# Kernel optimization log

Hardware: AMD Instinct MI355X
Metric: run time of the kernel (lower is better)

The kernel has to match this reference:

```python
import jax, jax.numpy as jnp
import numpy as np

N = 2048          # num nodes
C = 256           # dense_dim per input
EMB = 3 * C       # 768
H = 8             # num_heads
D = EMB // H      # 96 head_dim
ALPHA = 0.2       # leaky relu slope
SCALE = D ** -0.5


def setup_inputs() -> dict:
    key = jax.random.key(0)
    ks = jax.random.split(key, 9)
    sd = EMB ** -0.5
    return {
        "eh": jax.random.normal(ks[0], (N, C), jnp.float32),
        "er": jax.random.normal(ks[1], (N, C), jnp.float32),
        "et": jax.random.normal(ks[2], (N, C), jnp.float32),
        "h_id": jax.random.randint(ks[3], (N,), 0, 32),
        "W_w": jax.random.normal(ks[4], (EMB, EMB), jnp.float32) * sd,
        "a": jax.random.normal(ks[5], (2 * D, 1), jnp.float32) * (2 * D) ** -0.5,
        "proj_w": jax.random.normal(ks[6], (EMB, EMB), jnp.float32) * sd,
        "proj_b": jnp.zeros((EMB,), jnp.float32),
        "skip_w": jax.random.normal(ks[7], (EMB, EMB), jnp.float32) * sd,
        "skip_b": jnp.zeros((EMB,), jnp.float32),
    }


def reference(eh, er, et, h_id, W_w, a, proj_w, proj_b, skip_w, skip_b):
    n = eh.shape[0]
    e = jnp.concatenate([eh, er, et], axis=-1)            # [N, EMB]
    Wh = (e @ W_w.T).reshape(n, H, D)                     # [N, H, D]

    # score = leakyrelu(a1 . Wh_scrambled[i] + a2 . Wh[j]) * scale
    a1, a2 = a[:D, 0], a[D:, 0]
    s1 = Wh @ a1                                          # [N, H]
    s2 = Wh @ a2                                          # [N, H]
    # torch's Wh.repeat(1,1,N).view(N*N,H,D) reads head (j*H + h)//N for pair (i,j,h)
    qidx = (jnp.arange(n)[:, None] * H + jnp.arange(H)[None, :]) // n  # [N, H]
    x = s1[:, qidx] + s2[None, :, :]                      # [N, N, H]
    e_ij = jnp.where(x >= 0, x, ALPHA * x) * SCALE

    mask = h_id[:, None] != h_id[None, :]                 # [N, N]
    e_ij = jnp.where(mask[:, :, None], -jnp.inf, e_ij)
    attn = jax.nn.softmax(e_ij, axis=1)                   # softmax over neighbors j

    out = jnp.einsum('ijh,jhd->ihd', attn, Wh).reshape(n, H * D)
    out = out @ proj_w.T + proj_b                         # [N, EMB]
    skip = e @ skip_w.T + skip_b                          # [N, EMB]
    return skip + out
```

## Files before the change

### kernel.cpp

```cpp
#include <hip/hip_runtime.h>
#include <hip/hip_bf16.h>

#define N_NODES 2048
#define EMB 768
#define NH 8
#define DH 96
#define ALPHA 0.2f
#define SCALE 0.10206207261596575f

typedef __bf16 bf16x8 __attribute__((ext_vector_type(8)));
typedef float f32x4 __attribute__((ext_vector_type(4)));
typedef __attribute__((address_space(3))) unsigned int lds_u32;
typedef __attribute__((address_space(1))) const unsigned int glb_u32;

union pack4 { ushort4 u; __hip_bfloat16 h[4]; };

__global__ __launch_bounds__(256) void prep_kernel(
    const float* __restrict__ eh, const float* __restrict__ er, const float* __restrict__ et,
    const float* __restrict__ W0, const float* __restrict__ W1, const float* __restrict__ W2,
    __hip_bfloat16* __restrict__ e, __hip_bfloat16* __restrict__ o0,
    __hip_bfloat16* __restrict__ o1, __hip_bfloat16* __restrict__ o2, int* __restrict__ cnt)
{
    const int b = blockIdx.x;
    const int gtid = b * 256 + threadIdx.x;
    if (gtid < 32) cnt[gtid] = 0;
    const float* src;
    __hip_bfloat16* dst;
    if (b < 1536) {
        int idx = gtid * 4;
        int i = idx / EMB, c = idx % EMB;
        if (c < 256)      src = eh + i * 256 + c;
        else if (c < 512) src = er + i * 256 + (c - 256);
        else              src = et + i * 256 + (c - 512);
        dst = e + (size_t)i * EMB + c;
    } else {
        const int WSZ = EMB * EMB;
        int idx = (gtid - 1536 * 256) * 4;
        if (idx < WSZ)          { src = W0 + idx;           dst = o0 + idx; }
        else if (idx < 2 * WSZ) { src = W1 + idx - WSZ;     dst = o1 + idx - WSZ; }
        else                    { src = W2 + idx - 2 * WSZ; dst = o2 + idx - 2 * WSZ; }
    }
    float4 v = *reinterpret_cast<const float4*>(src);
    pack4 p;
    p.h[0] = __float2bfloat16(v.x);
    p.h[1] = __float2bfloat16(v.y);
    p.h[2] = __float2bfloat16(v.z);
    p.h[3] = __float2bfloat16(v.w);
    *reinterpret_cast<ushort4*>(dst) = p.u;
}

__device__ __forceinline__ void stage_tile(
    const __hip_bfloat16* __restrict__ src, int row0, int k0,
    __hip_bfloat16* lds, int wave, int lane)
{
#pragma unroll
    for (int r = 0; r < 2; r++) {
        const int L = wave * 128 + r * 64 + lane;
        const int row = L >> 3;
        const int cb = (L & 7) ^ (row & 7);
        const __hip_bfloat16* g = src + (size_t)(row0 + row) * EMB + k0 + cb * 8;
        __builtin_amdgcn_global_load_lds(
            (glb_u32*)g, (lds_u32*)(lds + (size_t)(wave * 128 + r * 64) * 8), 16, 0, 0);
    }
}

__global__ __launch_bounds__(256) void gemm_nt_kernel(
    const __hip_bfloat16* __restrict__ A1, const __hip_bfloat16* __restrict__ B1, int ns1,
    const __hip_bfloat16* __restrict__ A2, const __hip_bfloat16* __restrict__ B2, int ns2,
    const float* __restrict__ bias1, const float* __restrict__ bias2,
    float* __restrict__ Cf)
{
    __shared__ __attribute__((aligned(16))) __hip_bfloat16 sm[2][2][4096];

    const int t = threadIdx.x;
    const int lane = t & 63, wave = t >> 6;
    const int wm = wave >> 1, wn = wave & 1;
    const int bm = blockIdx.y * 64, bn = blockIdx.x * 64;
    const int l15 = lane & 15, quad = lane >> 4;
    const int NS = ns1 + ns2;

    f32x4 acc00 = {0.f,0.f,0.f,0.f}, acc01 = {0.f,0.f,0.f,0.f};
    f32x4 acc10 = {0.f,0.f,0.f,0.f}, acc11 = {0.f,0.f,0.f,0.f};

    stage_tile(A1, bm, 0, &sm[0][0][0], wave, lane);
    stage_tile(B1, bn, 0, &sm[0][1][0], wave, lane);

    const int rA = wm * 32 + l15;
    const int rB = wn * 32 + l15;
    const int xa = rA & 7, xb = rB & 7;

    for (int s = 0; s < NS; s++) {
        __syncthreads();
        if (s + 1 < NS) {
            const int sn = s + 1;
            const __hip_bfloat16* As = (sn < ns1) ? A1 : A2;
            const __hip_bfloat16* Bs = (sn < ns1) ? B1 : B2;
            const int k0 = ((sn < ns1) ? sn : sn - ns1) * 64;
            stage_tile(As, bm, k0, &sm[sn & 1][0][0], wave, lane);
            stage_tile(Bs, bn, k0, &sm[sn & 1][1][0], wave, lane);
        }
        const __hip_bfloat16* At = &sm[s & 1][0][0];
        const __hip_bfloat16* Bt = &sm[s & 1][1][0];
#pragma unroll
        for (int ks = 0; ks < 2; ks++) {
            const int cq = ks * 4 + quad;
            bf16x8 a0 = *(const bf16x8*)(At + ((size_t)rA        * 8 + (cq ^ xa)) * 8);
            bf16x8 a1 = *(const bf16x8*)(At + ((size_t)(rA + 16) * 8 + (cq ^ xa)) * 8);
            bf16x8 b0 = *(const bf16x8*)(Bt + ((size_t)rB        * 8 + (cq ^ xb)) * 8);
            bf16x8 b1 = *(const bf16x8*)(Bt + ((size_t)(rB + 16) * 8 + (cq ^ xb)) * 8);
            acc00 = __builtin_amdgcn_mfma_f32_16x16x32_bf16(a0, b0, acc00, 0, 0, 0);
            acc01 = __builtin_amdgcn_mfma_f32_16x16x32_bf16(a0, b1, acc01, 0, 0, 0);
            acc10 = __builtin_amdgcn_mfma_f32_16x16x32_bf16(a1, b0, acc10, 0, 0, 0);
            acc11 = __builtin_amdgcn_mfma_f32_16x16x32_bf16(a1, b1, acc11, 0, 0, 0);
        }
    }

    const int col0 = bn + wn * 32 + l15;
    const int col1 = col0 + 16;
    float bv0 = 0.f, bv1 = 0.f;
    if (bias1 != nullptr) {
        bv0 = bias1[col0] + bias2[col0];
        bv1 = bias1[col1] + bias2[col1];
    }
    const int r0 = bm + wm * 32 + quad * 4;
#pragma unroll
    for (int r = 0; r < 4; r++) {
        const int row0 = r0 + r, row1 = r0 + 16 + r;
        Cf[(size_t)row0 * EMB + col0] = acc00[r] + bv0;
        Cf[(size_t)row0 * EMB + col1] = acc01[r] + bv1;
        Cf[(size_t)row1 * EMB + col0] = acc10[r] + bv0;
        Cf[(size_t)row1 * EMB + col1] = acc11[r] + bv1;
    }
}

__global__ __launch_bounds__(256) void s12g_kernel(
    const float* __restrict__ Wh, const float* __restrict__ a,
    float* __restrict__ s1, float* __restrict__ s2,
    const int* __restrict__ h_id, int* __restrict__ cnt, int* __restrict__ lists)
{
    int gid = blockIdx.x * 256 + threadIdx.x;
    if (gid < N_NODES) {
        int g = h_id[gid];
        int p = atomicAdd(&cnt[g], 1);
        lists[g * N_NODES + p] = gid;
    }
    int i = gid >> 3, h = gid & 7;
    const float* wr = Wh + (size_t)i * EMB + h * DH;
    float acc1 = 0.f, acc2 = 0.f;
    for (int d = 0; d < DH; d++) {
        float w = wr[d];
        acc1 += w * a[d];
        acc2 += w * a[DH + d];
    }
    s1[gid] = acc1;
    s2[gid] = acc2;
}

__global__ __launch_bounds__(256) void attn_kernel(
    const float* __restrict__ Wh, const float* __restrict__ s1, const float* __restrict__ s2,
    const int* __restrict__ h_id, const int* __restrict__ cnt, const int* __restrict__ lists,
    __hip_bfloat16* __restrict__ out)
{
    const int i = blockIdx.x;
    const int t = threadIdx.x;
    const int lane = t & 63, wv = t >> 6;

    __shared__ float s1i[8];
    __shared__ float m_sh[8];
    __shared__ float S_sh[8];
    __shared__ float wred[4][8];
    __shared__ float wbuf[256][8];
    __shared__ int jbuf[256];

    const int g = h_id[i];
    const int ng = cnt[g];
    const int* gl = lists + g * N_NODES;

    if (t < 8) s1i[t] = s1[i * 8 + t];
    __syncthreads();

    float lv[8];
#pragma unroll
    for (int h = 0; h < 8; h++) lv[h] = -1e30f;
    for (int idx = t; idx < ng; idx += 256) {
        int j = gl[idx];
        float sq = s1i[j >> 8];
#pragma unroll
        for (int h = 0; h < 8; h++) {
            float x = sq + s2[j * 8 + h];
            float ev = (x >= 0.f ? x : ALPHA * x) * SCALE;
            lv[h] = fmaxf(lv[h], ev);
        }
    }
#pragma unroll
    for (int h = 0; h < 8; h++) {
        for (int o = 32; o > 0; o >>= 1) lv[h] = fmaxf(lv[h], __shfl_xor(lv[h], o));
    }
    if (lane == 0) {
#pragma unroll
        for (int h = 0; h < 8; h++) wred[wv][h] = lv[h];
    }
    __syncthreads();
    if (t < 8) m_sh[t] = fmaxf(fmaxf(wred[0][t], wred[1][t]), fmaxf(wred[2][t], wred[3][t]));
    __syncthreads();

#pragma unroll
    for (int h = 0; h < 8; h++) lv[h] = 0.f;
    for (int idx = t; idx < ng; idx += 256) {
        int j = gl[idx];
        float sq = s1i[j >> 8];
#pragma unroll
        for (int h = 0; h < 8; h++) {
            float x = sq + s2[j * 8 + h];
            float ev = (x >= 0.f ? x : ALPHA * x) * SCALE;
            lv[h] += __expf(ev - m_sh[h]);
        }
    }
#pragma unroll
    for (int h = 0; h < 8; h++) {
        for (int o = 32; o > 0; o >>= 1) lv[h] += __shfl_xor(lv[h], o);
    }
    if (lane == 0) {
#pragma unroll
        for (int h = 0; h < 8; h++) wred[wv][h] = lv[h];
    }
    __syncthreads();
    if (t < 8) S_sh[t] = 1.f / (wred[0][t] + wred[1][t] + wred[2][t] + wred[3][t]);
    __syncthreads();

    const int c0 = t, c1 = t + 256, c2 = t + 512;
    const int h0 = c0 / DH, h1 = c1 / DH, h2 = c2 / DH;
    float acc0 = 0.f, acc1 = 0.f, acc2 = 0.f;
    for (int base = 0; base < ng; base += 256) {
        const int cn = min(256, ng - base);
        __syncthreads();
        if (t < cn) {
            int j = gl[base + t];
            jbuf[t] = j;
            float sq = s1i[j >> 8];
#pragma unroll
            for (int h = 0; h < 8; h++) {
                float x = sq + s2[j * 8 + h];
                float ev = (x >= 0.f ? x : ALPHA * x) * SCALE;
                wbuf[t][h] = __expf(ev - m_sh[h]) * S_sh[h];
            }
        }
        __syncthreads();
        for (int c = 0; c < cn; c++) {
            const float* wr = Wh + (size_t)jbuf[c] * EMB;
            acc0 += wbuf[c][h0] * wr[c0];
            acc1 += wbuf[c][h1] * wr[c1];
            acc2 += wbuf[c][h2] * wr[c2];
        }
    }
    out[(size_t)i * EMB + c0] = __float2bfloat16(acc0);
    out[(size_t)i * EMB + c1] = __float2bfloat16(acc1);
    out[(size_t)i * EMB + c2] = __float2bfloat16(acc2);
}

extern "C" void kernel_launch(void* const* d_in, const int* in_sizes, int n_in,
                              void* d_out, int out_size, void* d_ws, size_t ws_size,
                              hipStream_t stream)
{
    const float* eh     = (const float*)d_in[0];
    const float* er     = (const float*)d_in[1];
    const float* et     = (const float*)d_in[2];
    const int*   h_id   = (const int*)d_in[3];
    const float* W_w    = (const float*)d_in[4];
    const float* a      = (const float*)d_in[5];
    const float* proj_w = (const float*)d_in[6];
    const float* proj_b = (const float*)d_in[7];
    const float* skip_w = (const float*)d_in[8];
    const float* skip_b = (const float*)d_in[9];
    float* out = (float*)d_out;

    char* ws = (char*)d_ws;
    __hip_bfloat16* e_ws   = (__hip_bfloat16*)(ws);
    float*          Wh_ws  = (float*)(ws + 3145728);
    __hip_bfloat16* at_ws  = (__hip_bfloat16*)(ws + 9437184);
    __hip_bfloat16* Wb_ws  = (__hip_bfloat16*)(ws + 12582912);
    __hip_bfloat16* Pb_ws  = (__hip_bfloat16*)(ws + 13762560);
    __hip_bfloat16* Sb_ws  = (__hip_bfloat16*)(ws + 14942208);
    float*          s1_ws  = (float*)(ws + 16121856);
    float*          s2_ws  = (float*)(ws + 16187392);
    int*            cnt_ws = (int*)(ws + 16252928);
    int*            lst_ws = (int*)(ws + 16253056);

    prep_kernel<<<3264, 256, 0, stream>>>(eh, er, et, W_w, proj_w, skip_w,
                                          e_ws, Wb_ws, Pb_ws, Sb_ws, cnt_ws);

    gemm_nt_kernel<<<dim3(12, 32), 256, 0, stream>>>(
        e_ws, Wb_ws, 12, nullptr, nullptr, 0, nullptr, nullptr, Wh_ws);

    s12g_kernel<<<64, 256, 0, stream>>>(Wh_ws, a, s1_ws, s2_ws, h_id, cnt_ws, lst_ws);

    attn_kernel<<<N_NODES, 256, 0, stream>>>(Wh_ws, s1_ws, s2_ws, h_id, cnt_ws, lst_ws, at_ws);

    gemm_nt_kernel<<<dim3(12, 32), 256, 0, stream>>>(
        at_ws, Pb_ws, 12, e_ws, Sb_ws, 12, proj_b, skip_b, out);
}
```

Measured before the change: 143.4 us.

## Restructure attention per group and head, staging group Wh slices in shared memory

```diff
diff --git a/kernel.cpp b/kernel.cpp
--- a/kernel.cpp
+++ b/kernel.cpp
@@ -7,6 +7,7 @@
 #define DH 96
 #define ALPHA 0.2f
 #define SCALE 0.10206207261596575f
+#define NGMAX 192
 
 typedef __bf16 bf16x8 __attribute__((ext_vector_type(8)));
 typedef float f32x4 __attribute__((ext_vector_type(4)));
@@ -158,104 +159,78 @@
 
 __global__ __launch_bounds__(256) void attn_kernel(
     const float* __restrict__ Wh, const float* __restrict__ s1, const float* __restrict__ s2,
-    const int* __restrict__ h_id, const int* __restrict__ cnt, const int* __restrict__ lists,
+    const int* __restrict__ cnt, const int* __restrict__ lists,
     __hip_bfloat16* __restrict__ out)
 {
-    const int i = blockIdx.x;
-    const int t = threadIdx.x;
-    const int lane = t & 63, wv = t >> 6;
-
-    __shared__ float s1i[8];
-    __shared__ float m_sh[8];
-    __shared__ float S_sh[8];
-    __shared__ float wred[4][8];
-    __shared__ float wbuf[256][8];
-    __shared__ int jbuf[256];
-
-    const int g = h_id[i];
-    const int ng = cnt[g];
+    const int g  = blockIdx.x & 31;
+    const int h  = (blockIdx.x >> 5) & 7;
+    const int dh = blockIdx.x >> 8;
+    const int t  = threadIdx.x;
+
+    __shared__ int   jb[NGMAX];
+    __shared__ int   qg[NGMAX];
+    __shared__ float s2g[NGMAX];
+    __shared__ float s1g[NGMAX][9];
+    __shared__ float Whg[NGMAX][48];
+
+    const int ng = min(cnt[g], NGMAX);
     const int* gl = lists + g * N_NODES;
 
-    if (t < 8) s1i[t] = s1[i * 8 + t];
+    for (int j = t; j < ng; j += 256) {
+        int node = gl[j];
+        jb[j]  = node;
+        qg[j]  = node >> 8;
+        s2g[j] = s2[node * 8 + h];
+        float4 v0 = *reinterpret_cast<const float4*>(s1 + node * 8);
+        float4 v1 = *reinterpret_cast<const float4*>(s1 + node * 8 + 4);
+        s1g[j][0] = v0.x; s1g[j][1] = v0.y; s1g[j][2] = v0.z; s1g[j][3] = v0.w;
+        s1g[j][4] = v1.x; s1g[j][5] = v1.y; s1g[j][6] = v1.z; s1g[j][7] = v1.w;
+    }
     __syncthreads();
-
-    float lv[8];
-#pragma unroll
-    for (int h = 0; h < 8; h++) lv[h] = -1e30f;
-    for (int idx = t; idx < ng; idx += 256) {
-        int j = gl[idx];
-        float sq = s1i[j >> 8];
-#pragma unroll
-        for (int h = 0; h < 8; h++) {
-            float x = sq + s2[j * 8 + h];
+    for (int idx = t; idx < ng * 12; idx += 256) {
+        int jc = idx / 12, dq = idx % 12;
+        float4 v = *reinterpret_cast<const float4*>(
+            Wh + (size_t)jb[jc] * EMB + h * DH + dh * 48 + dq * 4);
+        *reinterpret_cast<float4*>(&Whg[jc][dq * 4]) = v;
+    }
+    __syncthreads();
+
+    if (t < ng) {
+        float m = -1e30f;
+        for (int j = 0; j < ng; j++) {
+            float x = s1g[t][qg[j]] + s2g[j];
             float ev = (x >= 0.f ? x : ALPHA * x) * SCALE;
-            lv[h] = fmaxf(lv[h], ev);
-        }
-    }
-#pragma unroll
-    for (int h = 0; h < 8; h++) {
-        for (int o = 32; o > 0; o >>= 1) lv[h] = fmaxf(lv[h], __shfl_xor(lv[h], o));
-    }
-    if (lane == 0) {
-#pragma unroll
-        for (int h = 0; h < 8; h++) wred[wv][h] = lv[h];
-    }
-    __syncthreads();
-    if (t < 8) m_sh[t] = fmaxf(fmaxf(wred[0][t], wred[1][t]), fmaxf(wred[2][t], wred[3][t]));
-    __syncthreads();
-
-#pragma unroll
-    for (int h = 0; h < 8; h++) lv[h] = 0.f;
-    for (int idx = t; idx < ng; idx += 256) {
-        int j = gl[idx];
-        float sq = s1i[j >> 8];
-#pragma unroll
-        for (int h = 0; h < 8; h++) {
-            float x = sq + s2[j * 8 + h];
+            m = fmaxf(m, ev);
+        }
+        float S = 0.f;
+        for (int j = 0; j < ng; j++) {
+            float x = s1g[t][qg[j]] + s2g[j];
             float ev = (x >= 0.f ? x : ALPHA * x) * SCALE;
-            lv[h] += __expf(ev - m_sh[h]);
-        }
-    }
-#pragma unroll
-    for (int h = 0; h < 8; h++) {
-        for (int o = 32; o > 0; o >>= 1) lv[h] += __shfl_xor(lv[h], o);
-    }
-    if (lane == 0) {
-#pragma unroll
-        for (int h = 0; h < 8; h++) wred[wv][h] = lv[h];
-    }
-    __syncthreads();
-    if (t < 8) S_sh[t] = 1.f / (wred[0][t] + wred[1][t] + wred[2][t] + wred[3][t]);
-    __syncthreads();
-
-    const int c0 = t, c1 = t + 256, c2 = t + 512;
-    const int h0 = c0 / DH, h1 = c1 / DH, h2 = c2 / DH;
-    float acc0 = 0.f, acc1 = 0.f, acc2 = 0.f;
-    for (int base = 0; base < ng; base += 256) {
-        const int cn = min(256, ng - base);
-        __syncthreads();
-        if (t < cn) {
-            int j = gl[base + t];
-            jbuf[t] = j;
-            float sq = s1i[j >> 8];
-#pragma unroll
-            for (int h = 0; h < 8; h++) {
-                float x = sq + s2[j * 8 + h];
-                float ev = (x >= 0.f ? x : ALPHA * x) * SCALE;
-                wbuf[t][h] = __expf(ev - m_sh[h]) * S_sh[h];
-            }
-        }
-        __syncthreads();
-        for (int c = 0; c < cn; c++) {
-            const float* wr = Wh + (size_t)jbuf[c] * EMB;
-            acc0 += wbuf[c][h0] * wr[c0];
-            acc1 += wbuf[c][h1] * wr[c1];
-            acc2 += wbuf[c][h2] * wr[c2];
-        }
-    }
-    out[(size_t)i * EMB + c0] = __float2bfloat16(acc0);
-    out[(size_t)i * EMB + c1] = __float2bfloat16(acc1);
-    out[(size_t)i * EMB + c2] = __float2bfloat16(acc2);
+            S += __expf(ev - m);
+        }
+        const float ri = 1.f / S;
+
+        float acc[48];
+#pragma unroll
+        for (int d = 0; d < 48; d++) acc[d] = 0.f;
+        for (int j = 0; j < ng; j++) {
+            float x = s1g[t][qg[j]] + s2g[j];
+            float ev = (x >= 0.f ? x : ALPHA * x) * SCALE;
+            float p = __expf(ev - m) * ri;
+#pragma unroll
+            for (int d = 0; d < 48; d++) acc[d] += p * Whg[j][d];
+        }
+        __hip_bfloat16* po = out + (size_t)jb[t] * EMB + h * DH + dh * 48;
+#pragma unroll
+        for (int d = 0; d < 48; d += 4) {
+            pack4 pk;
+            pk.h[0] = __float2bfloat16(acc[d]);
+            pk.h[1] = __float2bfloat16(acc[d + 1]);
+            pk.h[2] = __float2bfloat16(acc[d + 2]);
+            pk.h[3] = __float2bfloat16(acc[d + 3]);
+            *reinterpret_cast<ushort4*>(po + d) = pk.u;
+        }
+    }
 }
 
 extern "C" void kernel_launch(void* const* d_in, const int* in_sizes, int n_in,
@@ -294,7 +269,7 @@
 
     s12g_kernel<<<64, 256, 0, stream>>>(Wh_ws, a, s1_ws, s2_ws, h_id, cnt_ws, lst_ws);
 
-    attn_kernel<<<N_NODES, 256, 0, stream>>>(Wh_ws, s1_ws, s2_ws, h_id, cnt_ws, lst_ws, at_ws);
+    attn_kernel<<<512, 256, 0, stream>>>(Wh_ws, s1_ws, s2_ws, cnt_ws, lst_ws, at_ws);
 
     gemm_nt_kernel<<<dim3(12, 32), 256, 0, stream>>>(
         at_ws, Pb_ws, 12, e_ws, Sb_ws, 12, proj_b, skip_b, out);
```

Result: no change. 142.3 us (-0.7%).
